# Performance work log

Measured on AMD Instinct MI355X. Metric: run time of the kernel, lower is better.

Reference implementation:

```python
import jax, jax.numpy as jnp
import numpy as np

HIDDEN = 4096
N_HEADS = 32
N_KV_HEADS = 8
HEAD_DIM = HIDDEN // N_HEADS  # 128
N_GROUPS = N_HEADS // N_KV_HEADS  # 4
ROPE_THETA = 10000.0
BSZ, SEQ = 2, 2048


def rotate_half(x):
    x1 = x[..., : x.shape[-1] // 2]
    x2 = x[..., x.shape[-1] // 2 :]
    return jnp.concatenate((-x2, x1), axis=-1)


def rope_tables(seq_len, head_dim, theta):
    inv_freq = 1.0 / theta ** (jnp.arange(0, head_dim, 2, dtype=jnp.float32) / head_dim)
    t = jnp.arange(seq_len, dtype=jnp.float32)
    freqs = jnp.einsum('i,j->ij', t, inv_freq)          # [S, head_dim/2]
    emb = jnp.concatenate((freqs, freqs), axis=-1)       # [S, head_dim]
    return jnp.cos(emb), jnp.sin(emb)


def setup_inputs() -> dict:
    key = jax.random.key(0)
    ks = jax.random.split(key, 5)
    hidden_states = jax.random.normal(ks[0], (BSZ, SEQ, HIDDEN), dtype=jnp.float32)
    # causal additive mask [B, 1, Q, K]
    causal = jnp.tril(jnp.ones((SEQ, SEQ), dtype=bool))
    attention_mask = jnp.where(causal, 0.0, -1e9).astype(jnp.float32)
    attention_mask = jnp.broadcast_to(attention_mask[None, None], (BSZ, 1, SEQ, SEQ))
    position_ids = jnp.broadcast_to(jnp.arange(SEQ, dtype=jnp.int32)[None, :], (BSZ, SEQ))
    sc = 1.0 / np.sqrt(HIDDEN)
    Wq = jax.random.normal(ks[1], (HIDDEN, N_HEADS * HEAD_DIM), dtype=jnp.float32) * sc
    Wk = jax.random.normal(ks[2], (HIDDEN, N_KV_HEADS * HEAD_DIM), dtype=jnp.float32) * sc
    Wv = jax.random.normal(ks[3], (HIDDEN, N_KV_HEADS * HEAD_DIM), dtype=jnp.float32) * sc
    Wo = jax.random.normal(ks[4], (N_HEADS * HEAD_DIM, HIDDEN), dtype=jnp.float32) * sc
    return {
        'hidden_states': hidden_states,
        'attention_mask': attention_mask,
        'position_ids': position_ids,
        'Wq': Wq, 'Wk': Wk, 'Wv': Wv, 'Wo': Wo,
    }


def reference(hidden_states, attention_mask, position_ids, Wq, Wk, Wv, Wo):
    bsz, q_len, _ = hidden_states.shape
    # QKV projections
    q = (hidden_states @ Wq).reshape(bsz, q_len, N_HEADS, HEAD_DIM).swapaxes(1, 2)       # [B,H,S,D]
    k = (hidden_states @ Wk).reshape(bsz, q_len, N_KV_HEADS, HEAD_DIM).swapaxes(1, 2)    # [B,Hkv,S,D]
    v = (hidden_states @ Wv).reshape(bsz, q_len, N_KV_HEADS, HEAD_DIM).swapaxes(1, 2)    # [B,Hkv,S,D]
    # RoPE
    cos_t, sin_t = rope_tables(q_len, HEAD_DIM, ROPE_THETA)
    cos = jnp.take(cos_t, position_ids, axis=0)[:, None]  # [B,1,S,D]
    sin = jnp.take(sin_t, position_ids, axis=0)[:, None]
    q = q * cos + rotate_half(q) * sin
    k = k * cos + rotate_half(k) * sin
    # GQA attention via grouped einsum (equivalent to repeat_kv, without materializing repeats)
    qg = q.reshape(bsz, N_KV_HEADS, N_GROUPS, q_len, HEAD_DIM)
    scores = jnp.einsum('bhgqd,bhkd->bhgqk', qg, k) / jnp.sqrt(jnp.float32(HEAD_DIM))
    scores = scores + attention_mask[:, :, None]  # broadcast mask over (kv_head, group)
    probs = jax.nn.softmax(scores.astype(jnp.float32), axis=-1).astype(hidden_states.dtype)
    out = jnp.einsum('bhgqk,bhkd->bhgqd', probs, v)
    out = out.reshape(bsz, N_HEADS, q_len, HEAD_DIM).swapaxes(1, 2).reshape(bsz, q_len, HIDDEN)
    return out @ Wo
```

## Files before the change

kernel.cpp:

```cpp
#include <hip/hip_runtime.h>
#include <hip/hip_bf16.h>
#include <cstdint>

#define HIDDEN 4096
#define NH 32
#define NKV 8
#define HD 128
#define SEQ 2048
#define BSZ 2
#define QKVN 6144
#define QKVLD 6144

using bf16x8 = __attribute__((ext_vector_type(8))) short;
using f32x4  = __attribute__((ext_vector_type(4))) float;

__device__ __forceinline__ ushort f2bf(float f) {
  union { float f; uint32_t u; } v; v.f = f;
  uint32_t r = (v.u + 0x7FFFu + ((v.u >> 16) & 1u)) >> 16;
  return (ushort)r;
}
__device__ __forceinline__ float bf2f(ushort s) {
  union { uint32_t u; float f; } v; v.u = ((uint32_t)s) << 16;
  return v.f;
}

__device__ __forceinline__ void gload_lds16(const void* g, void* l) {
  __builtin_amdgcn_global_load_lds(
      (const __attribute__((address_space(1))) void*)g,
      (__attribute__((address_space(3))) void*)l, 16, 0, 0);
}

__global__ __launch_bounds__(256)
void cvt_bf16_kernel(const float* __restrict__ X, ushort* __restrict__ Xb, int n8) {
  int t = blockIdx.x * 256 + threadIdx.x;
  if (t >= n8) return;
  size_t i = (size_t)t * 8;
  float4 a = *(const float4*)(X + i);
  float4 b = *(const float4*)(X + i + 4);
  uint4 p;
  p.x = (uint)f2bf(a.x) | ((uint)f2bf(a.y) << 16);
  p.y = (uint)f2bf(a.z) | ((uint)f2bf(a.w) << 16);
  p.z = (uint)f2bf(b.x) | ((uint)f2bf(b.y) << 16);
  p.w = (uint)f2bf(b.z) | ((uint)f2bf(b.w) << 16);
  *(uint4*)(Xb + i) = p;
}

__global__ __launch_bounds__(256)
void transpose_bf16_kernel(const float* __restrict__ W, ushort* __restrict__ WT,
                           int K, int N) {
  __shared__ ushort tile[32][33];
  const int k0 = blockIdx.y * 32, n0 = blockIdx.x * 32;
  const int tx = threadIdx.x & 31, ty = threadIdx.x >> 5;
  for (int i = 0; i < 4; ++i) {
    int k = ty + i * 8;
    tile[k][tx] = f2bf(W[(size_t)(k0 + k) * N + n0 + tx]);
  }
  __syncthreads();
  for (int i = 0; i < 4; ++i) {
    int n = ty + i * 8;
    WT[(size_t)(n0 + n) * K + k0 + tx] = tile[tx][n];
  }
}

template<int OUT_BF16>
__global__ __launch_bounds__(512, 2)
void gemm8p_kernel(const ushort* __restrict__ A, const ushort* __restrict__ BT,
                   void* __restrict__ Cp, int M, int N, int K) {
  extern __shared__ ushort lds[];
  const int tid = threadIdx.x, lane = tid & 63, wave = tid >> 6;
  const int l15 = lane & 15, l4 = lane >> 4;
  const int wr = wave >> 2, wc = wave & 3;

  const int mt = M >> 8, nt = N >> 8, nwg = mt * nt;
  const int swq = nwg >> 3, swr = nwg & 7;
  const int xcd = blockIdx.x & 7, lo = blockIdx.x >> 3;
  const int wg = (xcd < swr ? xcd * (swq + 1) : swr * (swq + 1) + (xcd - swr) * swq) + lo;
  const int m0 = (wg % mt) << 8;
  const int n0 = (wg / mt) << 8;

  ushort* LA[2][2];
  ushort* LB[2][2];
#pragma unroll
  for (int b_ = 0; b_ < 2; ++b_)
#pragma unroll
    for (int s_ = 0; s_ < 2; ++s_) {
      LA[b_][s_] = lds + ((b_ * 2 + 0) * 2 + s_) * 8192;
      LB[b_][s_] = lds + ((b_ * 2 + 1) * 2 + s_) * 8192;
    }

  const ushort* Abase = A + (size_t)m0 * K;
  const ushort* Bbase = BT + (size_t)n0 * K;

  const int srow0 = tid >> 2;
  const int scol8 = (((tid & 3) ^ ((srow0 >> 1) & 3)) << 3);

  const int swb  = (l4 ^ ((l15 >> 1) & 3)) << 3;
  const int aoff = (wr * 128 + l15) * 32 + swb;
  const int boff = (wc * 64 + l15) * 32 + swb;

  f32x4 acc[8][4] = {};
  bf16x8 a[8];
  bf16x8 b[4];

#define STAGE(buf, ks, kt, part)                                              \
  do {                                                                        \
    const size_t gc_ = (size_t)(kt) * 64 + (ks) * 32 + scol8;                 \
    const int rw_ = srow0 + (part) * 128;                                     \
    const int dst_ = ((part) * 512 + tid) * 8;                                \
    gload_lds16(Abase + (size_t)rw_ * K + gc_, &LA[buf][ks][dst_]);           \
    gload_lds16(Bbase + (size_t)rw_ * K + gc_, &LB[buf][ks][dst_]);           \
  } while (0)

#define MFMA_ __builtin_amdgcn_mfma_f32_16x16x32_bf16

#define PHASE_EVEN(buf, ks, sb, sk, skt)                                      \
  {                                                                           \
    _Pragma("unroll") for (int m_ = 0; m_ < 8; ++m_)                          \
      a[m_] = *(const bf16x8*)&LA[buf][ks][aoff + m_ * 512];                  \
    b[0] = *(const bf16x8*)&LB[buf][ks][boff];                                \
    b[1] = *(const bf16x8*)&LB[buf][ks][boff + 512];                          \
    STAGE(sb, sk, skt, 0);                                                    \
    asm volatile("s_barrier" ::: "memory");                                   \
    __builtin_amdgcn_s_setprio(1);                                            \
    _Pragma("unroll") for (int m_ = 0; m_ < 8; ++m_) {                        \
      acc[m_][0] = MFMA_(a[m_], b[0], acc[m_][0], 0, 0, 0);                   \
      acc[m_][1] = MFMA_(a[m_], b[1], acc[m_][1], 0, 0, 0);                   \
    }                                                                         \
    __builtin_amdgcn_s_setprio(0);                                            \
    asm volatile("s_barrier" ::: "memory");                                   \
  }

#define PHASE_ODD(buf, ks, sb, sk, skt)                                       \
  {                                                                           \
    b[2] = *(const bf16x8*)&LB[buf][ks][boff + 1024];                         \
    b[3] = *(const bf16x8*)&LB[buf][ks][boff + 1536];                         \
    STAGE(sb, sk, skt, 1);                                                    \
    asm volatile("s_barrier" ::: "memory");                                   \
    __builtin_amdgcn_s_setprio(1);                                            \
    _Pragma("unroll") for (int m_ = 0; m_ < 8; ++m_) {                        \
      acc[m_][2] = MFMA_(a[m_], b[2], acc[m_][2], 0, 0, 0);                   \
      acc[m_][3] = MFMA_(a[m_], b[3], acc[m_][3], 0, 0, 0);                   \
    }                                                                         \
    __builtin_amdgcn_s_setprio(0);                                            \
    asm volatile("s_waitcnt vmcnt(8)");                                       \
    asm volatile("s_barrier" ::: "memory");                                   \
  }

  const int NT = K >> 6;

  STAGE(0, 0, 0, 0); STAGE(0, 0, 0, 1);
  STAGE(0, 1, 0, 0); STAGE(0, 1, 0, 1);
  STAGE(1, 0, 1, 0); STAGE(1, 0, 1, 1);
  asm volatile("s_waitcnt vmcnt(8)");
  asm volatile("s_barrier" ::: "memory");

  for (int i = 0; i < (NT >> 1); ++i) {
    const int kt0 = 2 * i;
    const int ktA = (kt0 + 2 < NT) ? kt0 + 2 : NT - 1;
    const int ktB = (kt0 + 3 < NT) ? kt0 + 3 : NT - 1;
    PHASE_EVEN(0, 0, 1, 1, kt0 + 1)
    PHASE_ODD (0, 0, 1, 1, kt0 + 1)
    PHASE_EVEN(0, 1, 0, 0, ktA)
    PHASE_ODD (0, 1, 0, 0, ktA)
    PHASE_EVEN(1, 0, 0, 1, ktA)
    PHASE_ODD (1, 0, 0, 1, ktA)
    PHASE_EVEN(1, 1, 1, 0, ktB)
    PHASE_ODD (1, 1, 1, 0, ktB)
  }
#undef PHASE_EVEN
#undef PHASE_ODD
#undef STAGE

  const int crow0 = m0 + wr * 128 + l4 * 4;
  const int ccol0 = n0 + wc * 64 + l15;
#pragma unroll
  for (int m_ = 0; m_ < 8; ++m_)
#pragma unroll
    for (int n_ = 0; n_ < 4; ++n_)
#pragma unroll
      for (int r_ = 0; r_ < 4; ++r_) {
        const size_t row = crow0 + m_ * 16 + r_;
        const int col = ccol0 + n_ * 16;
        const float val = acc[m_][n_][r_];
        if (OUT_BF16) ((ushort*)Cp)[row * N + col] = f2bf(val);
        else          ((float*)Cp)[row * N + col]  = val;
      }
}

__global__ __launch_bounds__(256)
void rope_kernel(ushort* buf, const int* __restrict__ pos_ids, int nh, int ld, int total) {
  int t = blockIdx.x * 256 + threadIdx.x;
  if (t >= total) return;
  int j = t & 63;
  int rest = t >> 6;
  int h = rest % nh;
  int bs = rest / nh;
  float pos = (float)pos_ids[bs];
  float inv = exp2f(-(float)j * (13.287712379549449f / 64.0f));
  float ang = pos * inv;
  float c = cosf(ang), s = sinf(ang);
  ushort* p = buf + (size_t)bs * ld + h * HD + j;
  float x1 = bf2f(p[0]), x2 = bf2f(p[64]);
  p[0]  = f2bf(x1 * c - x2 * s);
  p[64] = f2bf(x2 * c + x1 * s);
}

__global__ __launch_bounds__(256)
void attn_kernel(const ushort* __restrict__ Q, const ushort* __restrict__ K0,
                 const ushort* __restrict__ V0, ushort* __restrict__ AO) {
  __shared__ ushort Ks[64 * 128];
  __shared__ ushort Vs[2][128 * 64];
  __shared__ ushort Ps[4][32 * 72];

  const int raw  = blockIdx.x;
  const int kh   = raw & 7;
  const int rest = raw >> 3;
  const int qt   = 63 - (rest & 63);
  const int b    = rest >> 6;
  const int q0   = qt * 32;

  const int tid = threadIdx.x, lane = tid & 63, wave = tid >> 6;
  const int l15 = lane & 15, l4 = lane >> 4;
  const int h = kh * 4 + wave;
  const float SCL2 = 0.1275173110f;

  const size_t bS = (size_t)b * SEQ;
  const ushort* Kb = K0 + bS * QKVLD + kh * HD;
  const ushort* Vb = V0 + bS * QKVLD + kh * HD;

  bf16x8 qf[2][4];
#pragma unroll
  for (int mi = 0; mi < 2; ++mi) {
    const ushort* qp = Q + (bS + q0 + mi * 16 + l15) * QKVLD + h * HD + l4 * 8;
#pragma unroll
    for (int kk = 0; kk < 4; ++kk) qf[mi][kk] = *(const bf16x8*)(qp + kk * 32);
  }

  float mrow[2][4], denom[2][4];
#pragma unroll
  for (int mi = 0; mi < 2; ++mi)
#pragma unroll
    for (int r = 0; r < 4; ++r) { mrow[mi][r] = -1e30f; denom[mi][r] = 0.0f; }
  f32x4 accO[2][8] = {};

  const int rp0 = tid & 31,        dc0 = tid >> 5;
  const int rp1 = (256 + tid) & 31, dc1 = (256 + tid) >> 5;

  const int nt = qt / 2 + 1;

  {
#pragma unroll
    for (int c = 0; c < 4; ++c) {
      const int j = wave * 4 + c;
      const int row = j * 4 + l4;
      const int chunk = (lane & 15) ^ (row & 7);
      gload_lds16(Kb + (size_t)row * QKVLD + chunk * 8, &Ks[j * 512 + lane * 8]);
    }
    const ushort* vp0 = Vb + (size_t)(2 * rp0) * QKVLD + dc0 * 8;
    const ushort* vp1 = Vb + (size_t)(2 * rp1) * QKVLD + dc1 * 8;
    bf16x8 lo0 = *(const bf16x8*)vp0, hi0 = *(const bf16x8*)(vp0 + QKVLD);
    bf16x8 lo1 = *(const bf16x8*)vp1, hi1 = *(const bf16x8*)(vp1 + QKVLD);
#pragma unroll
    for (int j = 0; j < 8; ++j) {
      const int d0 = dc0 * 8 + j, d1 = dc1 * 8 + j;
      uint v0p = (uint)(ushort)lo0[j] | ((uint)(ushort)hi0[j] << 16);
      uint v1p = (uint)(ushort)lo1[j] | ((uint)(ushort)hi1[j] << 16);
      *(uint*)&Vs[0][d0 * 64 + (((rp0 >> 2) ^ (d0 & 7)) << 3) + ((rp0 & 3) << 1)] = v0p;
      *(uint*)&Vs[0][d1 * 64 + (((rp1 >> 2) ^ (d1 & 7)) << 3) + ((rp1 & 3) << 1)] = v1p;
    }
  }
  __syncthreads();

  for (int t = 0; t < nt; ++t) {
    const int k0 = t * 64;
    const int cur = t & 1;
    const bool mask_tile = (t == nt - 1);
    const bool pf = (t + 1 < nt);

    f32x4 accS[2][4] = {};
    __builtin_amdgcn_s_setprio(1);
#pragma unroll
    for (int kk = 0; kk < 4; ++kk) {
#pragma unroll
      for (int ni = 0; ni < 4; ++ni) {
        bf16x8 kf = *(const bf16x8*)&Ks[(ni * 16 + l15) * 128 +
                                        (((kk * 4 + l4) ^ (l15 & 7)) << 3)];
        accS[0][ni] = __builtin_amdgcn_mfma_f32_16x16x32_bf16(qf[0][kk], kf, accS[0][ni], 0, 0, 0);
        accS[1][ni] = __builtin_amdgcn_mfma_f32_16x16x32_bf16(qf[1][kk], kf, accS[1][ni], 0, 0, 0);
      }
    }
    __builtin_amdgcn_s_setprio(0);
    __syncthreads();

    bf16x8 lo0, hi0, lo1, hi1;
    if (pf) {
      const int kn = k0 + 64;
#pragma unroll
      for (int c = 0; c < 4; ++c) {
        const int j = wave * 4 + c;
        const int row = j * 4 + l4;
        const int chunk = (lane & 15) ^ (row & 7);
        gload_lds16(Kb + (size_t)(kn + row) * QKVLD + chunk * 8, &Ks[j * 512 + lane * 8]);
      }
      const ushort* vp0 = Vb + (size_t)(kn + 2 * rp0) * QKVLD + dc0 * 8;
      const ushort* vp1 = Vb + (size_t)(kn + 2 * rp1) * QKVLD + dc1 * 8;
      lo0 = *(const bf16x8*)vp0; hi0 = *(const bf16x8*)(vp0 + QKVLD);
      lo1 = *(const bf16x8*)vp1; hi1 = *(const bf16x8*)(vp1 + QKVLD);
    }

    float pmax[2][4];
#pragma unroll
    for (int mi = 0; mi < 2; ++mi)
#pragma unroll
      for (int r = 0; r < 4; ++r) {
        float mx = -3e38f;
#pragma unroll
        for (int ni = 0; ni < 4; ++ni) {
          float x = accS[mi][ni][r] * SCL2;
          if (mask_tile) {
            int kq = k0 + ni * 16 + l15;
            int qq = q0 + mi * 16 + l4 * 4 + r;
            if (kq > qq) x = -1e30f;
          }
          accS[mi][ni][r] = x;
          mx = fmaxf(mx, x);
        }
        pmax[mi][r] = mx;
      }
#pragma unroll
    for (int d = 1; d < 16; d <<= 1)
#pragma unroll
      for (int mi = 0; mi < 2; ++mi)
#pragma unroll
        for (int r = 0; r < 4; ++r)
          pmax[mi][r] = fmaxf(pmax[mi][r], __shfl_xor(pmax[mi][r], d));

    bool ok = true;
#pragma unroll
    for (int mi = 0; mi < 2; ++mi)
#pragma unroll
      for (int r = 0; r < 4; ++r)
        ok = ok && (pmax[mi][r] - mrow[mi][r] <= 8.0f);

    if (__all(ok)) {
#pragma unroll
      for (int mi = 0; mi < 2; ++mi)
#pragma unroll
        for (int r = 0; r < 4; ++r) {
          const float mn = mrow[mi][r];
          float s = 0.0f;
#pragma unroll
          for (int ni = 0; ni < 4; ++ni) {
            float p = exp2f(accS[mi][ni][r] - mn);
            accS[mi][ni][r] = p;
            s += p;
          }
          denom[mi][r] += s;
        }
    } else {
#pragma unroll
      for (int mi = 0; mi < 2; ++mi)
#pragma unroll
        for (int r = 0; r < 4; ++r) {
          const float mn = fmaxf(mrow[mi][r], pmax[mi][r]);
          const float alpha = exp2f(mrow[mi][r] - mn);
          mrow[mi][r] = mn;
          float s = 0.0f;
#pragma unroll
          for (int ni = 0; ni < 4; ++ni) {
            float p = exp2f(accS[mi][ni][r] - mn);
            accS[mi][ni][r] = p;
            s += p;
          }
          denom[mi][r] = denom[mi][r] * alpha + s;
#pragma unroll
          for (int db = 0; db < 8; ++db) accO[mi][db][r] *= alpha;
        }
    }

#pragma unroll
    for (int mi = 0; mi < 2; ++mi)
#pragma unroll
      for (int ni = 0; ni < 4; ++ni)
#pragma unroll
        for (int r = 0; r < 4; ++r)
          Ps[wave][(mi * 16 + l4 * 4 + r) * 72 + ni * 16 + l15] = f2bf(accS[mi][ni][r]);

    __builtin_amdgcn_s_setprio(1);
#pragma unroll
    for (int kk = 0; kk < 2; ++kk) {
      bf16x8 pa[2];
#pragma unroll
      for (int mi = 0; mi < 2; ++mi)
        pa[mi] = *(const bf16x8*)&Ps[wave][(mi * 16 + l15) * 72 + kk * 32 + l4 * 8];
#pragma unroll
      for (int db = 0; db < 8; ++db) {
        bf16x8 vb = *(const bf16x8*)&Vs[cur][(db * 16 + l15) * 64 +
                                            (((kk * 4 + l4) ^ (l15 & 7)) << 3)];
        accO[0][db] = __builtin_amdgcn_mfma_f32_16x16x32_bf16(pa[0], vb, accO[0][db], 0, 0, 0);
        accO[1][db] = __builtin_amdgcn_mfma_f32_16x16x32_bf16(pa[1], vb, accO[1][db], 0, 0, 0);
      }
    }
    __builtin_amdgcn_s_setprio(0);

    if (pf) {
#pragma unroll
      for (int j = 0; j < 8; ++j) {
        const int d0 = dc0 * 8 + j, d1 = dc1 * 8 + j;
        uint v0p = (uint)(ushort)lo0[j] | ((uint)(ushort)hi0[j] << 16);
        uint v1p = (uint)(ushort)lo1[j] | ((uint)(ushort)hi1[j] << 16);
        *(uint*)&Vs[cur ^ 1][d0 * 64 + (((rp0 >> 2) ^ (d0 & 7)) << 3) + ((rp0 & 3) << 1)] = v0p;
        *(uint*)&Vs[cur ^ 1][d1 * 64 + (((rp1 >> 2) ^ (d1 & 7)) << 3) + ((rp1 & 3) << 1)] = v1p;
      }
    }
    __syncthreads();
  }

#pragma unroll
  for (int d = 1; d < 16; d <<= 1)
#pragma unroll
    for (int mi = 0; mi < 2; ++mi)
#pragma unroll
      for (int r = 0; r < 4; ++r)
        denom[mi][r] += __shfl_xor(denom[mi][r], d);

#pragma unroll
  for (int mi = 0; mi < 2; ++mi)
#pragma unroll
    for (int db = 0; db < 8; ++db)
#pragma unroll
      for (int r = 0; r < 4; ++r) {
        int q = q0 + mi * 16 + l4 * 4 + r;
        int col = h * HD + db * 16 + l15;
        AO[(bS + q) * HIDDEN + col] = f2bf(accO[mi][db][r] / denom[mi][r]);
      }
}

extern "C" void kernel_launch(void* const* d_in, const int* in_sizes, int n_in,
                              void* d_out, int out_size, void* d_ws, size_t ws_size,
                              hipStream_t stream) {
  (void)in_sizes; (void)n_in; (void)out_size; (void)ws_size;
  const float* X   = (const float*)d_in[0];
  const int*   pos = (const int*)d_in[2];
  const float* Wq  = (const float*)d_in[3];
  const float* Wk  = (const float*)d_in[4];
  const float* Wv  = (const float*)d_in[5];
  const float* Wo  = (const float*)d_in[6];

  char* ws = (char*)d_ws;
  ushort* Xb    = (ushort*)(ws);
  ushort* QKV   = (ushort*)(ws + 33554432);
  ushort* BTqkv = (ushort*)(ws + 83886080);
  ushort* WoT   = (ushort*)(ws + 134217728);
  ushort* AO    = Xb;

  const int M = BSZ * SEQ;
  dim3 blk(256);

  hipFuncSetAttribute((const void*)gemm8p_kernel<1>,
                      hipFuncAttributeMaxDynamicSharedMemorySize, 131072);
  hipFuncSetAttribute((const void*)gemm8p_kernel<0>,
                      hipFuncAttributeMaxDynamicSharedMemorySize, 131072);

  cvt_bf16_kernel<<<dim3((M * HIDDEN / 8 + 255) / 256), blk, 0, stream>>>(X, Xb, M * HIDDEN / 8);
  transpose_bf16_kernel<<<dim3(HIDDEN / 32, HIDDEN / 32), blk, 0, stream>>>(Wq, BTqkv, HIDDEN, HIDDEN);
  transpose_bf16_kernel<<<dim3((NKV * HD) / 32, HIDDEN / 32), blk, 0, stream>>>(
      Wk, BTqkv + (size_t)HIDDEN * HIDDEN, HIDDEN, NKV * HD);
  transpose_bf16_kernel<<<dim3((NKV * HD) / 32, HIDDEN / 32), blk, 0, stream>>>(
      Wv, BTqkv + (size_t)(HIDDEN + NKV * HD) * HIDDEN, HIDDEN, NKV * HD);
  transpose_bf16_kernel<<<dim3(HIDDEN / 32, HIDDEN / 32), blk, 0, stream>>>(Wo, WoT, HIDDEN, HIDDEN);

  gemm8p_kernel<1><<<dim3((M / 256) * (QKVN / 256)), dim3(512), 131072, stream>>>(
      Xb, BTqkv, QKV, M, QKVN, HIDDEN);

  rope_kernel<<<dim3((M * NH * 64) / 256), blk, 0, stream>>>(QKV, pos, NH, QKVLD, M * NH * 64);
  rope_kernel<<<dim3((M * NKV * 64) / 256), blk, 0, stream>>>(QKV + HIDDEN, pos, NKV, QKVLD, M * NKV * 64);

  attn_kernel<<<dim3(8 * 64 * BSZ), blk, 0, stream>>>(
      QKV, QKV + HIDDEN, QKV + HIDDEN + NKV * HD, AO);

  gemm8p_kernel<0><<<dim3((M / 256) * (HIDDEN / 256)), dim3(512), 131072, stream>>>(
      AO, WoT, d_out, M, HIDDEN, HIDDEN);
}
```

Measured before the change: 694.4 us.

## Pre-transpose V in global memory and load it asynchronously into LDS

Adds a kernel that transposes V into a per-(batch, kv-head) [D, S] layout in the workspace. Attention can then fetch V tiles with direct global-to-LDS loads instead of register loads followed by packed LDS stores. This removes the register staging and scatter stores from the attention loop, at the cost of an extra kernel launch and an extra pass over V. It also moves the row-max shuffle reduction into the rescale branch, so it runs only when the wave-level fast-path check fails.

```diff
diff --git a/kernel.cpp b/kernel.cpp
--- a/kernel.cpp
+++ b/kernel.cpp
@@ -59,6 +59,26 @@
   for (int i = 0; i < 4; ++i) {
     int n = ty + i * 8;
     WT[(size_t)(n0 + n) * K + k0 + tx] = tile[tx][n];
+  }
+}
+
+__global__ __launch_bounds__(256)
+void transpose_v_kernel(const ushort* __restrict__ Vsrc, ushort* __restrict__ VtG) {
+  __shared__ ushort tile[32][33];
+  const int slice = blockIdx.z;
+  const int b = slice >> 3, kh = slice & 7;
+  const int s0 = blockIdx.x * 32, d0 = blockIdx.y * 32;
+  const int tx = threadIdx.x & 31, ty = threadIdx.x >> 5;
+  const ushort* src = Vsrc + ((size_t)(b * SEQ) + s0) * QKVLD + kh * HD + d0;
+  for (int i = 0; i < 4; ++i) {
+    int s = ty + i * 8;
+    tile[s][tx] = src[(size_t)s * QKVLD + tx];
+  }
+  __syncthreads();
+  ushort* dst = VtG + ((size_t)slice * HD + d0) * SEQ + s0;
+  for (int i = 0; i < 4; ++i) {
+    int d = ty + i * 8;
+    dst[(size_t)d * SEQ + tx] = tile[tx][d];
   }
 }
 
@@ -207,7 +227,7 @@
 
 __global__ __launch_bounds__(256)
 void attn_kernel(const ushort* __restrict__ Q, const ushort* __restrict__ K0,
-                 const ushort* __restrict__ V0, ushort* __restrict__ AO) {
+                 const ushort* __restrict__ VtG, ushort* __restrict__ AO) {
   __shared__ ushort Ks[64 * 128];
   __shared__ ushort Vs[2][128 * 64];
   __shared__ ushort Ps[4][32 * 72];
@@ -226,7 +246,10 @@
 
   const size_t bS = (size_t)b * SEQ;
   const ushort* Kb = K0 + bS * QKVLD + kh * HD;
-  const ushort* Vb = V0 + bS * QKVLD + kh * HD;
+  const ushort* Vb = VtG + (size_t)(b * NKV + kh) * HD * SEQ;
+
+  const int vrow = lane >> 3;
+  const int vslot = lane & 7;
 
   bf16x8 qf[2][4];
 #pragma unroll
@@ -242,9 +265,6 @@
 #pragma unroll
     for (int r = 0; r < 4; ++r) { mrow[mi][r] = -1e30f; denom[mi][r] = 0.0f; }
   f32x4 accO[2][8] = {};
-
-  const int rp0 = tid & 31,        dc0 = tid >> 5;
-  const int rp1 = (256 + tid) & 31, dc1 = (256 + tid) >> 5;
 
   const int nt = qt / 2 + 1;
 
@@ -253,20 +273,15 @@
     for (int c = 0; c < 4; ++c) {
       const int j = wave * 4 + c;
       const int row = j * 4 + l4;
-      const int chunk = (lane & 15) ^ (row & 7);
+      const int chunk = l15 ^ (row & 7);
       gload_lds16(Kb + (size_t)row * QKVLD + chunk * 8, &Ks[j * 512 + lane * 8]);
     }
-    const ushort* vp0 = Vb + (size_t)(2 * rp0) * QKVLD + dc0 * 8;
-    const ushort* vp1 = Vb + (size_t)(2 * rp1) * QKVLD + dc1 * 8;
-    bf16x8 lo0 = *(const bf16x8*)vp0, hi0 = *(const bf16x8*)(vp0 + QKVLD);
-    bf16x8 lo1 = *(const bf16x8*)vp1, hi1 = *(const bf16x8*)(vp1 + QKVLD);
-#pragma unroll
-    for (int j = 0; j < 8; ++j) {
-      const int d0 = dc0 * 8 + j, d1 = dc1 * 8 + j;
-      uint v0p = (uint)(ushort)lo0[j] | ((uint)(ushort)hi0[j] << 16);
-      uint v1p = (uint)(ushort)lo1[j] | ((uint)(ushort)hi1[j] << 16);
-      *(uint*)&Vs[0][d0 * 64 + (((rp0 >> 2) ^ (d0 & 7)) << 3) + ((rp0 & 3) << 1)] = v0p;
-      *(uint*)&Vs[0][d1 * 64 + (((rp1 >> 2) ^ (d1 & 7)) << 3) + ((rp1 & 3) << 1)] = v1p;
+#pragma unroll
+    for (int c = 0; c < 4; ++c) {
+      const int j = wave * 4 + c;
+      const int d = j * 8 + vrow;
+      const int chunk = vslot ^ (d & 7);
+      gload_lds16(Vb + (size_t)d * SEQ + chunk * 8, &Vs[0][j * 512 + lane * 8]);
     }
   }
   __syncthreads();
@@ -292,20 +307,23 @@
     __builtin_amdgcn_s_setprio(0);
     __syncthreads();
 
-    bf16x8 lo0, hi0, lo1, hi1;
     if (pf) {
       const int kn = k0 + 64;
 #pragma unroll
       for (int c = 0; c < 4; ++c) {
         const int j = wave * 4 + c;
         const int row = j * 4 + l4;
-        const int chunk = (lane & 15) ^ (row & 7);
+        const int chunk = l15 ^ (row & 7);
         gload_lds16(Kb + (size_t)(kn + row) * QKVLD + chunk * 8, &Ks[j * 512 + lane * 8]);
       }
-      const ushort* vp0 = Vb + (size_t)(kn + 2 * rp0) * QKVLD + dc0 * 8;
-      const ushort* vp1 = Vb + (size_t)(kn + 2 * rp1) * QKVLD + dc1 * 8;
-      lo0 = *(const bf16x8*)vp0; hi0 = *(const bf16x8*)(vp0 + QKVLD);
-      lo1 = *(const bf16x8*)vp1; hi1 = *(const bf16x8*)(vp1 + QKVLD);
+#pragma unroll
+      for (int c = 0; c < 4; ++c) {
+        const int j = wave * 4 + c;
+        const int d = j * 8 + vrow;
+        const int chunk = vslot ^ (d & 7);
+        gload_lds16(Vb + (size_t)d * SEQ + kn + chunk * 8,
+                    &Vs[cur ^ 1][j * 512 + lane * 8]);
+      }
     }
 
     float pmax[2][4];
@@ -327,13 +345,6 @@
         }
         pmax[mi][r] = mx;
       }
-#pragma unroll
-    for (int d = 1; d < 16; d <<= 1)
-#pragma unroll
-      for (int mi = 0; mi < 2; ++mi)
-#pragma unroll
-        for (int r = 0; r < 4; ++r)
-          pmax[mi][r] = fmaxf(pmax[mi][r], __shfl_xor(pmax[mi][r], d));
 
     bool ok = true;
 #pragma unroll
@@ -359,6 +370,13 @@
         }
     } else {
 #pragma unroll
+      for (int d = 1; d < 16; d <<= 1)
+#pragma unroll
+        for (int mi = 0; mi < 2; ++mi)
+#pragma unroll
+          for (int r = 0; r < 4; ++r)
+            pmax[mi][r] = fmaxf(pmax[mi][r], __shfl_xor(pmax[mi][r], d));
+#pragma unroll
       for (int mi = 0; mi < 2; ++mi)
 #pragma unroll
         for (int r = 0; r < 4; ++r) {
@@ -403,16 +421,6 @@
     }
     __builtin_amdgcn_s_setprio(0);
 
-    if (pf) {
-#pragma unroll
-      for (int j = 0; j < 8; ++j) {
-        const int d0 = dc0 * 8 + j, d1 = dc1 * 8 + j;
-        uint v0p = (uint)(ushort)lo0[j] | ((uint)(ushort)hi0[j] << 16);
-        uint v1p = (uint)(ushort)lo1[j] | ((uint)(ushort)hi1[j] << 16);
-        *(uint*)&Vs[cur ^ 1][d0 * 64 + (((rp0 >> 2) ^ (d0 & 7)) << 3) + ((rp0 & 3) << 1)] = v0p;
-        *(uint*)&Vs[cur ^ 1][d1 * 64 + (((rp1 >> 2) ^ (d1 & 7)) << 3) + ((rp1 & 3) << 1)] = v1p;
-      }
-    }
     __syncthreads();
   }
 
@@ -453,6 +461,7 @@
   ushort* BTqkv = (ushort*)(ws + 83886080);
   ushort* WoT   = (ushort*)(ws + 134217728);
   ushort* AO    = Xb;
+  ushort* VtG   = BTqkv;
 
   const int M = BSZ * SEQ;
   dim3 blk(256);
@@ -475,9 +484,10 @@
 
   rope_kernel<<<dim3((M * NH * 64) / 256), blk, 0, stream>>>(QKV, pos, NH, QKVLD, M * NH * 64);
   rope_kernel<<<dim3((M * NKV * 64) / 256), blk, 0, stream>>>(QKV + HIDDEN, pos, NKV, QKVLD, M * NKV * 64);
-
-  attn_kernel<<<dim3(8 * 64 * BSZ), blk, 0, stream>>>(
-      QKV, QKV + HIDDEN, QKV + HIDDEN + NKV * HD, AO);
+  transpose_v_kernel<<<dim3(SEQ / 32, HD / 32, BSZ * NKV), blk, 0, stream>>>(
+      QKV + HIDDEN + NKV * HD, VtG);
+
+  attn_kernel<<<dim3(8 * 64 * BSZ), blk, 0, stream>>>(QKV, QKV + HIDDEN, VtG, AO);
 
   gemm8p_kernel<0><<<dim3((M / 256) * (HIDDEN / 256)), dim3(512), 131072, stream>>>(
       AO, WoT, d_out, M, HIDDEN, HIDDEN);
```

Result: faster. 639.1 us (-8.0%).
